# Performance work log

Hardware: AMD Instinct MI355X
Metric: run time of the kernel (lower is better)

The kernel has to match this reference:

```python
import jax, jax.numpy as jnp
import numpy as np

TEMPERATURE = 0.07
COS_EPS = 1e-8  # torch F.cosine_similarity clamps norms at eps=1e-8


def setup_inputs() -> dict:
    key = jax.random.key(0)
    features = jax.random.normal(key, (8192, 1024), dtype=jnp.float32)
    return {"features": features}


def reference(features):
    n = features.shape[0]
    b = n // 2
    # Cosine similarity as normalize + GEMM (equivalent to broadcasted F.cosine_similarity)
    norms = jnp.maximum(jnp.linalg.norm(features, axis=1, keepdims=True), COS_EPS)
    fn = features / norms                      # [N, D]
    sim = (fn @ fn.T) / TEMPERATURE            # [N, N]
    # Mask self-similarity on the diagonal with -inf
    diag = jnp.eye(n, dtype=bool)
    sim = jnp.where(diag, -jnp.inf, sim)
    # labels: positive of i is its paired augmentation (i+b mod n)
    labels = jnp.concatenate([jnp.arange(b) + b, jnp.arange(b)])  # [N]
    # Cross-entropy in one stable pass
    log_probs = jax.nn.log_softmax(sim, axis=1)
    loss = -jnp.mean(log_probs[jnp.arange(n), labels])
    return loss
```

## Files before the change

kernel.cpp:

```cpp
#include <hip/hip_runtime.h>
#include <hip/hip_bf16.h>

#define N_ROWS 8192
#define D_DIM  1024
#define HALF_N 4096
#define N_TILES 2080
#define N_RED  8
constexpr float INV_T = 1.0f / 0.07f;

typedef __attribute__((ext_vector_type(4))) float f32x4;
typedef __attribute__((ext_vector_type(2))) long long2_;

__device__ __forceinline__ void async_ld16(const void* g, void* lds) {
    __builtin_amdgcn_global_load_lds(
        (const __attribute__((address_space(1))) void*)g,
        (__attribute__((address_space(3))) void*)lds,
        16, 0, 0);
}

__device__ __forceinline__ unsigned int pk_fp8x4(float a, float b, float c, float d) {
    int v = __builtin_amdgcn_cvt_pk_fp8_f32(a, b, 0, false);
    v = __builtin_amdgcn_cvt_pk_fp8_f32(c, d, v, true);
    return (unsigned int)v;
}

__global__ __launch_bounds__(256) void norm_kernel(const float* __restrict__ feat,
                                                   unsigned char* __restrict__ fn8,
                                                   float* __restrict__ row_sum,
                                                   unsigned int* __restrict__ done_cnt,
                                                   unsigned int* __restrict__ fin_cnt,
                                                   float* __restrict__ loss_acc) {
    const int w = threadIdx.x >> 6, lane = threadIdx.x & 63;
    const int row = blockIdx.x * 4 + w;
    if (blockIdx.x == 0 && threadIdx.x == 0) {
        *done_cnt = 0u;
        *fin_cnt = 0u;
        *loss_acc = 0.f;
    }
    const float4* src = (const float4*)(feat + (size_t)row * D_DIM);
    float4 v[4];
    float ss = 0.f;
#pragma unroll
    for (int t = 0; t < 4; ++t) {
        v[t] = src[lane + 64 * t];
        ss += v[t].x * v[t].x + v[t].y * v[t].y + v[t].z * v[t].z + v[t].w * v[t].w;
    }
#pragma unroll
    for (int off = 32; off; off >>= 1) ss += __shfl_xor(ss, off);
    float nrm = fmaxf(sqrtf(ss), 1e-8f);
    if (lane == 0) row_sum[row] = 0.f;
    const float inv = 1.0f / nrm;
    unsigned int* dst = (unsigned int*)(fn8 + (size_t)row * D_DIM);
#pragma unroll
    for (int t = 0; t < 4; ++t)
        dst[lane + 64 * t] = pk_fp8x4(v[t].x * inv, v[t].y * inv, v[t].z * inv, v[t].w * inv);
}

__global__ __launch_bounds__(256) void simgemm_kernel(const unsigned char* __restrict__ fn8,
                                                      float* __restrict__ row_sum,
                                                      float* __restrict__ s_target,
                                                      unsigned int* __restrict__ done_cnt,
                                                      unsigned int* __restrict__ fin_cnt,
                                                      float* __restrict__ loss_acc,
                                                      float* __restrict__ out) {
    __shared__ __align__(16) unsigned char As[128 * 64];
    __shared__ __align__(16) unsigned char Bs[128 * 64];
    const int t = blockIdx.x;
    int a = (int)((sqrtf(8.f * (float)t + 1.f) - 1.f) * 0.5f);
    while ((a + 1) * (a + 2) / 2 <= t) ++a;
    while (a * (a + 1) / 2 > t) --a;
    const int I = t - a * (a + 1) / 2;
    const int J = a;
    const int r0 = I * 128, c0 = J * 128;
    const bool isdiag = (I == J);
    const bool haspair = (J == I + 32);

    const int tid = threadIdx.x;
    const int w = tid >> 6, lane = tid & 63;
    const int q = lane >> 4, c16 = lane & 15;
    const int wr = (w >> 1) * 64;
    const int wc = (w & 1) * 64;
    const int wr4 = (w >> 1) * 4;
    const int wc4 = (w & 1) * 4;
    const int srow = lane >> 2;
    const int skoff = ((lane & 3) ^ ((srow >> 1) & 3)) * 16;
    const int lfo = c16 * 64 + ((q ^ ((c16 >> 1) & 3)) * 16);

    const unsigned char* pa0 = fn8 + (size_t)(r0 + w * 32 + srow) * D_DIM + skoff;
    const unsigned char* pa1 = pa0 + 16 * D_DIM;
    const unsigned char* pb0 = fn8 + (size_t)(c0 + w * 32 + srow) * D_DIM + skoff;
    const unsigned char* pb1 = pb0 + 16 * D_DIM;

    f32x4 acc[4][4];
#pragma unroll
    for (int i = 0; i < 4; ++i)
#pragma unroll
        for (int j = 0; j < 4; ++j) acc[i][j] = (f32x4){0.f, 0.f, 0.f, 0.f};

    for (int kt = 0; kt < 16; ++kt) {
        __syncthreads();
        async_ld16(pa0, (void*)&As[(w * 2 + 0) * 1024]);
        async_ld16(pa1, (void*)&As[(w * 2 + 1) * 1024]);
        async_ld16(pb0, (void*)&Bs[(w * 2 + 0) * 1024]);
        async_ld16(pb1, (void*)&Bs[(w * 2 + 1) * 1024]);
        pa0 += 64; pa1 += 64; pb0 += 64; pb1 += 64;
        __syncthreads();

        long2_ af[4], bf[4];
#pragma unroll
        for (int i = 0; i < 4; ++i)
            af[i] = *(const long2_*)&As[(wr4 + i) * 1024 + lfo];
#pragma unroll
        for (int j = 0; j < 4; ++j)
            bf[j] = *(const long2_*)&Bs[(wc4 + j) * 1024 + lfo];
#pragma unroll
        for (int i = 0; i < 4; ++i)
#pragma unroll
            for (int j = 0; j < 4; ++j) {
                acc[i][j] = __builtin_amdgcn_mfma_f32_16x16x32_fp8_fp8(
                    af[i].x, bf[j].x, acc[i][j], 0, 0, 0);
                acc[i][j] = __builtin_amdgcn_mfma_f32_16x16x32_fp8_fp8(
                    af[i].y, bf[j].y, acc[i][j], 0, 0, 0);
            }
    }

    float cs[4] = {0.f, 0.f, 0.f, 0.f};
#pragma unroll
    for (int i = 0; i < 4; ++i) {
        const int growb = r0 + wr + i * 16 + q * 4;
#pragma unroll
        for (int r = 0; r < 4; ++r) {
            const int grow = growb + r;
            float s = 0.f;
#pragma unroll
            for (int j = 0; j < 4; ++j) {
                const int gcol = c0 + wc + j * 16 + c16;
                float sim = acc[i][j][r] * INV_T;
                float e = __expf(sim - INV_T);
                if (isdiag && grow == gcol) e = 0.f;
                if (haspair && gcol == grow + HALF_N) {
                    __hip_atomic_store(&s_target[grow], sim, __ATOMIC_RELAXED,
                                       __HIP_MEMORY_SCOPE_AGENT);
                    __hip_atomic_store(&s_target[gcol], sim, __ATOMIC_RELAXED,
                                       __HIP_MEMORY_SCOPE_AGENT);
                }
                s += e;
                cs[j] += e;
            }
            s += __shfl_xor(s, 1);
            s += __shfl_xor(s, 2);
            s += __shfl_xor(s, 4);
            s += __shfl_xor(s, 8);
            if (c16 == 0) atomicAdd(&row_sum[grow], s);
        }
    }
    if (!isdiag) {
#pragma unroll
        for (int j = 0; j < 4; ++j) {
            float s = cs[j];
            s += __shfl_xor(s, 16);
            s += __shfl_xor(s, 32);
            if (q == 0) atomicAdd(&row_sum[c0 + wc + j * 16 + c16], s);
        }
    }

    __syncthreads();
    __shared__ unsigned int my_ord;
    if (tid == 0)
        my_ord = __hip_atomic_fetch_add(done_cnt, 1u, __ATOMIC_RELAXED,
                                        __HIP_MEMORY_SCOPE_AGENT);
    __syncthreads();
    const unsigned int ord = my_ord;
    if (ord >= N_TILES - N_RED) {
        if (tid == 0) {
            while (__hip_atomic_load(done_cnt, __ATOMIC_RELAXED,
                                     __HIP_MEMORY_SCOPE_AGENT) < N_TILES)
                __builtin_amdgcn_s_sleep(1);
        }
        __syncthreads();
        const int slice = (int)(ord - (N_TILES - N_RED));
        const int base_row = slice * (N_ROWS / N_RED) + tid * 4;
        float rv[4], sv[4];
#pragma unroll
        for (int u = 0; u < 4; ++u) {
            rv[u] = __hip_atomic_load(&row_sum[base_row + u], __ATOMIC_RELAXED,
                                      __HIP_MEMORY_SCOPE_AGENT);
            sv[u] = __hip_atomic_load(&s_target[base_row + u], __ATOMIC_RELAXED,
                                      __HIP_MEMORY_SCOPE_AGENT);
        }
        float local = 0.f;
#pragma unroll
        for (int u = 0; u < 4; ++u)
            local += __logf(rv[u]) - sv[u];
#pragma unroll
        for (int off = 32; off; off >>= 1) local += __shfl_xor(local, off);
        __shared__ float part[4];
        if ((tid & 63) == 0) part[tid >> 6] = local;
        __syncthreads();
        if (tid == 0) {
            float bsum = part[0] + part[1] + part[2] + part[3];
            __hip_atomic_fetch_add(loss_acc, bsum, __ATOMIC_RELAXED,
                                   __HIP_MEMORY_SCOPE_AGENT);
            unsigned int f = __hip_atomic_fetch_add(fin_cnt, 1u, __ATOMIC_ACQ_REL,
                                                    __HIP_MEMORY_SCOPE_AGENT);
            if (f == N_RED - 1) {
                float accv = __hip_atomic_load(loss_acc, __ATOMIC_RELAXED,
                                               __HIP_MEMORY_SCOPE_AGENT);
                out[0] = INV_T + accv * (1.0f / N_ROWS);
            }
        }
    }
}

extern "C" void kernel_launch(void* const* d_in, const int* in_sizes, int n_in,
                              void* d_out, int out_size, void* d_ws, size_t ws_size,
                              hipStream_t stream) {
    const float* feat = (const float*)d_in[0];
    float* out = (float*)d_out;
    char* ws = (char*)d_ws;

    unsigned char* fn8 = (unsigned char*)ws;
    size_t off = (size_t)N_ROWS * D_DIM;
    float* row_sum = (float*)(ws + off);   off += N_ROWS * sizeof(float);
    float* s_target = (float*)(ws + off);  off += N_ROWS * sizeof(float);
    unsigned int* done_cnt = (unsigned int*)(ws + off);  off += sizeof(unsigned int);
    unsigned int* fin_cnt = (unsigned int*)(ws + off);   off += sizeof(unsigned int);
    float* loss_acc = (float*)(ws + off);

    norm_kernel<<<N_ROWS / 4, 256, 0, stream>>>(feat, fn8, row_sum, done_cnt, fin_cnt, loss_acc);
    simgemm_kernel<<<N_TILES, 256, 0, stream>>>(fn8, row_sum, s_target, done_cnt, fin_cnt, loss_acc, out);
}
```

Measured before the change: 142.7 us.

## Use 128x256 tiles with triple-buffered async LDS pipeline and 8 waves

Each block now computes a 128x256 tile of the upper-triangular similarity matrix with 512 threads, so the grid shrinks from 2080 to 1056 blocks. Tile masking is rewritten to handle rectangular tiles that straddle the diagonal. The K loop is software-pipelined with three LDS buffers, raw barriers and explicit waitcnts, and setprio is raised around the MFMA bursts so loads overlap with compute. The aim is fewer barriers per MFMA and hidden global-load latency. The cost is more LDS per block and harder-to-verify synchronisation, and the diagonal tiles do some redundant work.

```diff
diff --git a/kernel.cpp b/kernel.cpp
--- a/kernel.cpp
+++ b/kernel.cpp
@@ -4,7 +4,7 @@
 #define N_ROWS 8192
 #define D_DIM  1024
 #define HALF_N 4096
-#define N_TILES 2080
+#define N_TILES 1056
 #define N_RED  8
 constexpr float INV_T = 1.0f / 0.07f;
 
@@ -56,38 +56,52 @@
         dst[lane + 64 * t] = pk_fp8x4(v[t].x * inv, v[t].y * inv, v[t].z * inv, v[t].w * inv);
 }
 
-__global__ __launch_bounds__(256) void simgemm_kernel(const unsigned char* __restrict__ fn8,
-                                                      float* __restrict__ row_sum,
-                                                      float* __restrict__ s_target,
-                                                      unsigned int* __restrict__ done_cnt,
-                                                      unsigned int* __restrict__ fin_cnt,
-                                                      float* __restrict__ loss_acc,
-                                                      float* __restrict__ out) {
-    __shared__ __align__(16) unsigned char As[128 * 64];
-    __shared__ __align__(16) unsigned char Bs[128 * 64];
+#define BARRIER() do { asm volatile("" ::: "memory"); \
+    __builtin_amdgcn_s_barrier();                      \
+    asm volatile("" ::: "memory"); } while (0)
+
+#define MROW(AF, I_) do { \
+    acc[I_][0] = __builtin_amdgcn_mfma_f32_16x16x32_fp8_fp8(AF.x, bf[0].x, acc[I_][0], 0, 0, 0); \
+    acc[I_][1] = __builtin_amdgcn_mfma_f32_16x16x32_fp8_fp8(AF.x, bf[1].x, acc[I_][1], 0, 0, 0); \
+    acc[I_][2] = __builtin_amdgcn_mfma_f32_16x16x32_fp8_fp8(AF.x, bf[2].x, acc[I_][2], 0, 0, 0); \
+    acc[I_][3] = __builtin_amdgcn_mfma_f32_16x16x32_fp8_fp8(AF.x, bf[3].x, acc[I_][3], 0, 0, 0); \
+    acc[I_][0] = __builtin_amdgcn_mfma_f32_16x16x32_fp8_fp8(AF.y, bf[0].y, acc[I_][0], 0, 0, 0); \
+    acc[I_][1] = __builtin_amdgcn_mfma_f32_16x16x32_fp8_fp8(AF.y, bf[1].y, acc[I_][1], 0, 0, 0); \
+    acc[I_][2] = __builtin_amdgcn_mfma_f32_16x16x32_fp8_fp8(AF.y, bf[2].y, acc[I_][2], 0, 0, 0); \
+    acc[I_][3] = __builtin_amdgcn_mfma_f32_16x16x32_fp8_fp8(AF.y, bf[3].y, acc[I_][3], 0, 0, 0); \
+} while (0)
+
+__global__ __launch_bounds__(512, 4) void simgemm_kernel(const unsigned char* __restrict__ fn8,
+                                                         float* __restrict__ row_sum,
+                                                         float* __restrict__ s_target,
+                                                         unsigned int* __restrict__ done_cnt,
+                                                         unsigned int* __restrict__ fin_cnt,
+                                                         float* __restrict__ loss_acc,
+                                                         float* __restrict__ out) {
+    __shared__ __align__(16) unsigned char As[3][8 * 1024];
+    __shared__ __align__(16) unsigned char Bs[3][16 * 1024];
+
     const int t = blockIdx.x;
-    int a = (int)((sqrtf(8.f * (float)t + 1.f) - 1.f) * 0.5f);
-    while ((a + 1) * (a + 2) / 2 <= t) ++a;
-    while (a * (a + 1) / 2 > t) --a;
-    const int I = t - a * (a + 1) / 2;
-    const int J = a;
-    const int r0 = I * 128, c0 = J * 128;
-    const bool isdiag = (I == J);
-    const bool haspair = (J == I + 32);
+#define CSUM(i) (32 * (i) - ((i) >> 1) * (((i) - 1) >> 1))
+    int I = 64 - (int)sqrtf(fmaxf(4096.f - 4.f * (float)t, 0.f)) - 2;
+    if (I < 0) I = 0;
+    if (I > 63) I = 63;
+    while (CSUM(I + 1) <= t) ++I;
+    while (CSUM(I) > t) --I;
+    const int J = (I >> 1) + (t - CSUM(I));
+    const int r0 = I * 128, c0 = J * 256;
+    const bool haspair = (J == (I >> 1) + (HALF_N / 256));
 
     const int tid = threadIdx.x;
     const int w = tid >> 6, lane = tid & 63;
     const int q = lane >> 4, c16 = lane & 15;
-    const int wr = (w >> 1) * 64;
-    const int wc = (w & 1) * 64;
-    const int wr4 = (w >> 1) * 4;
-    const int wc4 = (w & 1) * 4;
+    const int wm = w >> 2, wn = w & 3;
+    const int wm4 = wm * 4, wn4 = wn * 4;
     const int srow = lane >> 2;
     const int skoff = ((lane & 3) ^ ((srow >> 1) & 3)) * 16;
     const int lfo = c16 * 64 + ((q ^ ((c16 >> 1) & 3)) * 16);
 
-    const unsigned char* pa0 = fn8 + (size_t)(r0 + w * 32 + srow) * D_DIM + skoff;
-    const unsigned char* pa1 = pa0 + 16 * D_DIM;
+    const unsigned char* pa  = fn8 + (size_t)(r0 + w * 16 + srow) * D_DIM + skoff;
     const unsigned char* pb0 = fn8 + (size_t)(c0 + w * 32 + srow) * D_DIM + skoff;
     const unsigned char* pb1 = pb0 + 16 * D_DIM;
 
@@ -97,47 +111,75 @@
 #pragma unroll
         for (int j = 0; j < 4; ++j) acc[i][j] = (f32x4){0.f, 0.f, 0.f, 0.f};
 
+    async_ld16(pa,       &As[0][w * 1024]);
+    async_ld16(pb0,      &Bs[0][(2 * w) * 1024]);
+    async_ld16(pb1,      &Bs[0][(2 * w + 1) * 1024]);
+    async_ld16(pa  + 64, &As[1][w * 1024]);
+    async_ld16(pb0 + 64, &Bs[1][(2 * w) * 1024]);
+    async_ld16(pb1 + 64, &Bs[1][(2 * w + 1) * 1024]);
+    pa += 128; pb0 += 128; pb1 += 128;
+    asm volatile("s_waitcnt vmcnt(3)" ::: "memory");
+    BARRIER();
+
+    int cur = 0;
     for (int kt = 0; kt < 16; ++kt) {
-        __syncthreads();
-        async_ld16(pa0, (void*)&As[(w * 2 + 0) * 1024]);
-        async_ld16(pa1, (void*)&As[(w * 2 + 1) * 1024]);
-        async_ld16(pb0, (void*)&Bs[(w * 2 + 0) * 1024]);
-        async_ld16(pb1, (void*)&Bs[(w * 2 + 1) * 1024]);
-        pa0 += 64; pa1 += 64; pb0 += 64; pb1 += 64;
-        __syncthreads();
-
-        long2_ af[4], bf[4];
-#pragma unroll
-        for (int i = 0; i < 4; ++i)
-            af[i] = *(const long2_*)&As[(wr4 + i) * 1024 + lfo];
-#pragma unroll
-        for (int j = 0; j < 4; ++j)
-            bf[j] = *(const long2_*)&Bs[(wc4 + j) * 1024 + lfo];
-#pragma unroll
-        for (int i = 0; i < 4; ++i)
-#pragma unroll
-            for (int j = 0; j < 4; ++j) {
-                acc[i][j] = __builtin_amdgcn_mfma_f32_16x16x32_fp8_fp8(
-                    af[i].x, bf[j].x, acc[i][j], 0, 0, 0);
-                acc[i][j] = __builtin_amdgcn_mfma_f32_16x16x32_fp8_fp8(
-                    af[i].y, bf[j].y, acc[i][j], 0, 0, 0);
-            }
+        const bool pre = (kt < 14);
+        int nb = cur + 2; if (nb >= 3) nb -= 3;
+        long2_ bf[4], a0, a1;
+        bf[0] = *(const long2_*)&Bs[cur][(wn4 + 0) * 1024 + lfo];
+        bf[1] = *(const long2_*)&Bs[cur][(wn4 + 1) * 1024 + lfo];
+        bf[2] = *(const long2_*)&Bs[cur][(wn4 + 2) * 1024 + lfo];
+        bf[3] = *(const long2_*)&Bs[cur][(wn4 + 3) * 1024 + lfo];
+        a0 = *(const long2_*)&As[cur][(wm4 + 0) * 1024 + lfo];
+        a1 = *(const long2_*)&As[cur][(wm4 + 1) * 1024 + lfo];
+        if (pre) {
+            async_ld16(pa,  &As[nb][w * 1024]);
+            async_ld16(pb0, &Bs[nb][(2 * w) * 1024]);
+        }
+        BARRIER();
+        asm volatile("s_waitcnt lgkmcnt(0)" ::: "memory");
+        __builtin_amdgcn_s_setprio(1);
+        MROW(a0, 0);
+        MROW(a1, 1);
+        __builtin_amdgcn_s_setprio(0);
+        BARRIER();
+        a0 = *(const long2_*)&As[cur][(wm4 + 2) * 1024 + lfo];
+        a1 = *(const long2_*)&As[cur][(wm4 + 3) * 1024 + lfo];
+        if (pre) {
+            async_ld16(pb1, &Bs[nb][(2 * w + 1) * 1024]);
+            pa += 64; pb0 += 64; pb1 += 64;
+        }
+        BARRIER();
+        asm volatile("s_waitcnt lgkmcnt(0)" ::: "memory");
+        __builtin_amdgcn_s_setprio(1);
+        MROW(a0, 2);
+        MROW(a1, 3);
+        __builtin_amdgcn_s_setprio(0);
+        if (kt < 14) {
+            asm volatile("s_waitcnt vmcnt(3)" ::: "memory");
+            BARRIER();
+        } else if (kt == 14) {
+            asm volatile("s_waitcnt vmcnt(0)" ::: "memory");
+            BARRIER();
+        }
+        cur = (cur == 2) ? 0 : cur + 1;
     }
 
     float cs[4] = {0.f, 0.f, 0.f, 0.f};
 #pragma unroll
     for (int i = 0; i < 4; ++i) {
-        const int growb = r0 + wr + i * 16 + q * 4;
+        const int growb = r0 + wm * 64 + i * 16 + q * 4;
 #pragma unroll
         for (int r = 0; r < 4; ++r) {
             const int grow = growb + r;
             float s = 0.f;
 #pragma unroll
             for (int j = 0; j < 4; ++j) {
-                const int gcol = c0 + wc + j * 16 + c16;
+                const int gcol = c0 + wn * 64 + j * 16 + c16;
                 float sim = acc[i][j][r] * INV_T;
                 float e = __expf(sim - INV_T);
-                if (isdiag && grow == gcol) e = 0.f;
+                const bool same128 = (((grow ^ gcol) >> 7) == 0);
+                if (grow == gcol || (!same128 && grow > gcol)) e = 0.f;
                 if (haspair && gcol == grow + HALF_N) {
                     __hip_atomic_store(&s_target[grow], sim, __ATOMIC_RELAXED,
                                        __HIP_MEMORY_SCOPE_AGENT);
@@ -145,7 +187,7 @@
                                        __HIP_MEMORY_SCOPE_AGENT);
                 }
                 s += e;
-                cs[j] += e;
+                cs[j] += same128 ? 0.f : e;
             }
             s += __shfl_xor(s, 1);
             s += __shfl_xor(s, 2);
@@ -154,14 +196,12 @@
             if (c16 == 0) atomicAdd(&row_sum[grow], s);
         }
     }
-    if (!isdiag) {
-#pragma unroll
-        for (int j = 0; j < 4; ++j) {
-            float s = cs[j];
-            s += __shfl_xor(s, 16);
-            s += __shfl_xor(s, 32);
-            if (q == 0) atomicAdd(&row_sum[c0 + wc + j * 16 + c16], s);
-        }
+#pragma unroll
+    for (int j = 0; j < 4; ++j) {
+        float s = cs[j];
+        s += __shfl_xor(s, 16);
+        s += __shfl_xor(s, 32);
+        if (q == 0) atomicAdd(&row_sum[c0 + wn * 64 + j * 16 + c16], s);
     }
 
     __syncthreads();
@@ -179,26 +219,25 @@
         }
         __syncthreads();
         const int slice = (int)(ord - (N_TILES - N_RED));
-        const int base_row = slice * (N_ROWS / N_RED) + tid * 4;
-        float rv[4], sv[4];
-#pragma unroll
-        for (int u = 0; u < 4; ++u) {
-            rv[u] = __hip_atomic_load(&row_sum[base_row + u], __ATOMIC_RELAXED,
-                                      __HIP_MEMORY_SCOPE_AGENT);
-            sv[u] = __hip_atomic_load(&s_target[base_row + u], __ATOMIC_RELAXED,
-                                      __HIP_MEMORY_SCOPE_AGENT);
-        }
-        float local = 0.f;
-#pragma unroll
-        for (int u = 0; u < 4; ++u)
-            local += __logf(rv[u]) - sv[u];
+        const int base_row = slice * (N_ROWS / N_RED) + tid * 2;
+        float rv0 = __hip_atomic_load(&row_sum[base_row + 0], __ATOMIC_RELAXED,
+                                      __HIP_MEMORY_SCOPE_AGENT);
+        float rv1 = __hip_atomic_load(&row_sum[base_row + 1], __ATOMIC_RELAXED,
+                                      __HIP_MEMORY_SCOPE_AGENT);
+        float sv0 = __hip_atomic_load(&s_target[base_row + 0], __ATOMIC_RELAXED,
+                                      __HIP_MEMORY_SCOPE_AGENT);
+        float sv1 = __hip_atomic_load(&s_target[base_row + 1], __ATOMIC_RELAXED,
+                                      __HIP_MEMORY_SCOPE_AGENT);
+        float local = __logf(rv0) - sv0 + __logf(rv1) - sv1;
 #pragma unroll
         for (int off = 32; off; off >>= 1) local += __shfl_xor(local, off);
-        __shared__ float part[4];
-        if ((tid & 63) == 0) part[tid >> 6] = local;
+        __shared__ float part[8];
+        if ((tid & 63) == 0) part[w] = local;
         __syncthreads();
         if (tid == 0) {
-            float bsum = part[0] + part[1] + part[2] + part[3];
+            float bsum = 0.f;
+#pragma unroll
+            for (int k = 0; k < 8; ++k) bsum += part[k];
             __hip_atomic_fetch_add(loss_acc, bsum, __ATOMIC_RELAXED,
                                    __HIP_MEMORY_SCOPE_AGENT);
             unsigned int f = __hip_atomic_fetch_add(fin_cnt, 1u, __ATOMIC_ACQ_REL,
@@ -228,5 +267,5 @@
     float* loss_acc = (float*)(ws + off);
 
     norm_kernel<<<N_ROWS / 4, 256, 0, stream>>>(feat, fn8, row_sum, done_cnt, fin_cnt, loss_acc);
-    simgemm_kernel<<<N_TILES, 256, 0, stream>>>(fn8, row_sum, s_target, done_cnt, fin_cnt, loss_acc, out);
-}
+    simgemm_kernel<<<N_TILES, 512, 0, stream>>>(fn8, row_sum, s_target, done_cnt, fin_cnt, loss_acc, out);
+}
```

New measurement: 153.6 us. +7.6%, slower.

## Triple-buffer LDS tiles with async prefetch and split MFMA phases

Applied to the files above, without the earlier changes.

Replaces the single-buffered LDS load/compute loop with a three-stage ring buffer that keeps two k-tiles of async global-to-LDS loads in flight, with manual vmcnt waits and one barrier per iteration instead of two. The MFMA work is split into two half phases with interleaved LDS fragment reads and raised wave priority, and occupancy is hinted via launch bounds. This aims to hide global load latency behind the matrix math. It triples LDS use per block, which may limit occupancy, and depends on hand-written waitcnt correctness.

```diff
diff --git a/kernel.cpp b/kernel.cpp
--- a/kernel.cpp
+++ b/kernel.cpp
@@ -56,15 +56,30 @@
         dst[lane + 64 * t] = pk_fp8x4(v[t].x * inv, v[t].y * inv, v[t].z * inv, v[t].w * inv);
 }
 
-__global__ __launch_bounds__(256) void simgemm_kernel(const unsigned char* __restrict__ fn8,
-                                                      float* __restrict__ row_sum,
-                                                      float* __restrict__ s_target,
-                                                      unsigned int* __restrict__ done_cnt,
-                                                      unsigned int* __restrict__ fin_cnt,
-                                                      float* __restrict__ loss_acc,
-                                                      float* __restrict__ out) {
-    __shared__ __align__(16) unsigned char As[128 * 64];
-    __shared__ __align__(16) unsigned char Bs[128 * 64];
+#define BARRIER() do { asm volatile("" ::: "memory"); \
+    __builtin_amdgcn_s_barrier();                      \
+    asm volatile("" ::: "memory"); } while (0)
+
+#define MROW(AF, I_) do { \
+    acc[I_][0] = __builtin_amdgcn_mfma_f32_16x16x32_fp8_fp8(AF.x, bf[0].x, acc[I_][0], 0, 0, 0); \
+    acc[I_][1] = __builtin_amdgcn_mfma_f32_16x16x32_fp8_fp8(AF.x, bf[1].x, acc[I_][1], 0, 0, 0); \
+    acc[I_][2] = __builtin_amdgcn_mfma_f32_16x16x32_fp8_fp8(AF.x, bf[2].x, acc[I_][2], 0, 0, 0); \
+    acc[I_][3] = __builtin_amdgcn_mfma_f32_16x16x32_fp8_fp8(AF.x, bf[3].x, acc[I_][3], 0, 0, 0); \
+    acc[I_][0] = __builtin_amdgcn_mfma_f32_16x16x32_fp8_fp8(AF.y, bf[0].y, acc[I_][0], 0, 0, 0); \
+    acc[I_][1] = __builtin_amdgcn_mfma_f32_16x16x32_fp8_fp8(AF.y, bf[1].y, acc[I_][1], 0, 0, 0); \
+    acc[I_][2] = __builtin_amdgcn_mfma_f32_16x16x32_fp8_fp8(AF.y, bf[2].y, acc[I_][2], 0, 0, 0); \
+    acc[I_][3] = __builtin_amdgcn_mfma_f32_16x16x32_fp8_fp8(AF.y, bf[3].y, acc[I_][3], 0, 0, 0); \
+} while (0)
+
+__global__ __launch_bounds__(256, 3) void simgemm_kernel(const unsigned char* __restrict__ fn8,
+                                                         float* __restrict__ row_sum,
+                                                         float* __restrict__ s_target,
+                                                         unsigned int* __restrict__ done_cnt,
+                                                         unsigned int* __restrict__ fin_cnt,
+                                                         float* __restrict__ loss_acc,
+                                                         float* __restrict__ out) {
+    __shared__ __align__(16) unsigned char As[3][8 * 1024];
+    __shared__ __align__(16) unsigned char Bs[3][8 * 1024];
     const int t = blockIdx.x;
     int a = (int)((sqrtf(8.f * (float)t + 1.f) - 1.f) * 0.5f);
     while ((a + 1) * (a + 2) / 2 <= t) ++a;
@@ -97,31 +112,54 @@
 #pragma unroll
         for (int j = 0; j < 4; ++j) acc[i][j] = (f32x4){0.f, 0.f, 0.f, 0.f};
 
+    async_ld16(pa0,      &As[0][(w * 2 + 0) * 1024]);
+    async_ld16(pa1,      &As[0][(w * 2 + 1) * 1024]);
+    async_ld16(pb0,      &Bs[0][(w * 2 + 0) * 1024]);
+    async_ld16(pb1,      &Bs[0][(w * 2 + 1) * 1024]);
+    async_ld16(pa0 + 64, &As[1][(w * 2 + 0) * 1024]);
+    async_ld16(pa1 + 64, &As[1][(w * 2 + 1) * 1024]);
+    async_ld16(pb0 + 64, &Bs[1][(w * 2 + 0) * 1024]);
+    async_ld16(pb1 + 64, &Bs[1][(w * 2 + 1) * 1024]);
+    asm volatile("s_waitcnt vmcnt(4)" ::: "memory");
+    BARRIER();
+
+    int cur = 0;
     for (int kt = 0; kt < 16; ++kt) {
-        __syncthreads();
-        async_ld16(pa0, (void*)&As[(w * 2 + 0) * 1024]);
-        async_ld16(pa1, (void*)&As[(w * 2 + 1) * 1024]);
-        async_ld16(pb0, (void*)&Bs[(w * 2 + 0) * 1024]);
-        async_ld16(pb1, (void*)&Bs[(w * 2 + 1) * 1024]);
-        pa0 += 64; pa1 += 64; pb0 += 64; pb1 += 64;
-        __syncthreads();
-
-        long2_ af[4], bf[4];
-#pragma unroll
-        for (int i = 0; i < 4; ++i)
-            af[i] = *(const long2_*)&As[(wr4 + i) * 1024 + lfo];
-#pragma unroll
-        for (int j = 0; j < 4; ++j)
-            bf[j] = *(const long2_*)&Bs[(wc4 + j) * 1024 + lfo];
-#pragma unroll
-        for (int i = 0; i < 4; ++i)
-#pragma unroll
-            for (int j = 0; j < 4; ++j) {
-                acc[i][j] = __builtin_amdgcn_mfma_f32_16x16x32_fp8_fp8(
-                    af[i].x, bf[j].x, acc[i][j], 0, 0, 0);
-                acc[i][j] = __builtin_amdgcn_mfma_f32_16x16x32_fp8_fp8(
-                    af[i].y, bf[j].y, acc[i][j], 0, 0, 0);
-            }
+        int nb = cur + 2; if (nb >= 3) nb -= 3;
+        long2_ bf[4], a0, a1;
+        bf[0] = *(const long2_*)&Bs[cur][(wc4 + 0) * 1024 + lfo];
+        bf[1] = *(const long2_*)&Bs[cur][(wc4 + 1) * 1024 + lfo];
+        bf[2] = *(const long2_*)&Bs[cur][(wc4 + 2) * 1024 + lfo];
+        bf[3] = *(const long2_*)&Bs[cur][(wc4 + 3) * 1024 + lfo];
+        a0 = *(const long2_*)&As[cur][(wr4 + 0) * 1024 + lfo];
+        a1 = *(const long2_*)&As[cur][(wr4 + 1) * 1024 + lfo];
+        if (kt < 14) {
+            const int off = (kt + 2) * 64;
+            async_ld16(pa0 + off, &As[nb][(w * 2 + 0) * 1024]);
+            async_ld16(pa1 + off, &As[nb][(w * 2 + 1) * 1024]);
+            async_ld16(pb0 + off, &Bs[nb][(w * 2 + 0) * 1024]);
+            async_ld16(pb1 + off, &Bs[nb][(w * 2 + 1) * 1024]);
+        }
+        asm volatile("s_waitcnt lgkmcnt(0)" ::: "memory");
+        __builtin_amdgcn_s_setprio(1);
+        MROW(a0, 0);
+        MROW(a1, 1);
+        __builtin_amdgcn_s_setprio(0);
+        a0 = *(const long2_*)&As[cur][(wr4 + 2) * 1024 + lfo];
+        a1 = *(const long2_*)&As[cur][(wr4 + 3) * 1024 + lfo];
+        asm volatile("s_waitcnt lgkmcnt(0)" ::: "memory");
+        __builtin_amdgcn_s_setprio(1);
+        MROW(a0, 2);
+        MROW(a1, 3);
+        __builtin_amdgcn_s_setprio(0);
+        if (kt < 14) {
+            asm volatile("s_waitcnt vmcnt(4)" ::: "memory");
+            BARRIER();
+        } else if (kt == 14) {
+            asm volatile("s_waitcnt vmcnt(0)" ::: "memory");
+            BARRIER();
+        }
+        cur = (cur == 2) ? 0 : cur + 1;
     }
 
     float cs[4] = {0.f, 0.f, 0.f, 0.f};
```

After: 142.2 us. No clear change (-0.4%).

## Switch FP8 GEMM to 32x32x64 scaled MFMA with 128-wide K tiles

Applied to the files above, without the earlier changes.

Replaces the 16x16x32 fp8 MFMA tiles with the gfx950 mfma_scale 32x32x64 f8f6f4 instruction (unit scales), changes the per-wave accumulator layout to 2x2 32x32 tiles and doubles the K step per LDS stage to 128 bytes with a new XOR swizzle. This halves the number of barrier-separated K iterations and cuts MFMA instruction count, aiming at higher matrix throughput. The epilogue reductions are rewritten for the 32x32 output layout, which risks layout or swizzle errors and raises LDS use to 32KB.

```diff
diff --git a/kernel.cpp b/kernel.cpp
--- a/kernel.cpp
+++ b/kernel.cpp
@@ -8,8 +8,10 @@
 #define N_RED  8
 constexpr float INV_T = 1.0f / 0.07f;
 
-typedef __attribute__((ext_vector_type(4))) float f32x4;
-typedef __attribute__((ext_vector_type(2))) long long2_;
+typedef __attribute__((ext_vector_type(4)))  float f32x4;
+typedef __attribute__((ext_vector_type(16))) float f32x16;
+typedef __attribute__((ext_vector_type(4)))  int   i32x4;
+typedef __attribute__((ext_vector_type(8)))  int   i32x8;
 
 __device__ __forceinline__ void async_ld16(const void* g, void* lds) {
     __builtin_amdgcn_global_load_lds(
@@ -23,6 +25,18 @@
     v = __builtin_amdgcn_cvt_pk_fp8_f32(c, d, v, true);
     return (unsigned int)v;
 }
+
+__device__ __forceinline__ i32x8 ld_frag(const unsigned char* rowbase, int lo, int hi) {
+    i32x4 L = *(const i32x4*)(rowbase + lo);
+    i32x4 H = *(const i32x4*)(rowbase + hi);
+    i32x8 r;
+    r[0] = L[0]; r[1] = L[1]; r[2] = L[2]; r[3] = L[3];
+    r[4] = H[0]; r[5] = H[1]; r[6] = H[2]; r[7] = H[3];
+    return r;
+}
+
+#define MXMFMA(AF, BF, ACC) ACC = __builtin_amdgcn_mfma_scale_f32_32x32x64_f8f6f4( \
+        AF, BF, ACC, 0, 0, 0, 0x7F7F7F7F, 0, 0x7F7F7F7F)
 
 __global__ __launch_bounds__(256) void norm_kernel(const float* __restrict__ feat,
                                                    unsigned char* __restrict__ fn8,
@@ -63,8 +77,8 @@
                                                       unsigned int* __restrict__ fin_cnt,
                                                       float* __restrict__ loss_acc,
                                                       float* __restrict__ out) {
-    __shared__ __align__(16) unsigned char As[128 * 64];
-    __shared__ __align__(16) unsigned char Bs[128 * 64];
+    __shared__ __align__(16) unsigned char As[128 * 128];
+    __shared__ __align__(16) unsigned char Bs[128 * 128];
     const int t = blockIdx.x;
     int a = (int)((sqrtf(8.f * (float)t + 1.f) - 1.f) * 0.5f);
     while ((a + 1) * (a + 2) / 2 <= t) ++a;
@@ -77,65 +91,62 @@
 
     const int tid = threadIdx.x;
     const int w = tid >> 6, lane = tid & 63;
-    const int q = lane >> 4, c16 = lane & 15;
     const int wr = (w >> 1) * 64;
     const int wc = (w & 1) * 64;
-    const int wr4 = (w >> 1) * 4;
-    const int wc4 = (w & 1) * 4;
-    const int srow = lane >> 2;
-    const int skoff = ((lane & 3) ^ ((srow >> 1) & 3)) * 16;
-    const int lfo = c16 * 64 + ((q ^ ((c16 >> 1) & 3)) * 16);
-
-    const unsigned char* pa0 = fn8 + (size_t)(r0 + w * 32 + srow) * D_DIM + skoff;
-    const unsigned char* pa1 = pa0 + 16 * D_DIM;
-    const unsigned char* pb0 = fn8 + (size_t)(c0 + w * 32 + srow) * D_DIM + skoff;
-    const unsigned char* pb1 = pb0 + 16 * D_DIM;
-
-    f32x4 acc[4][4];
-#pragma unroll
-    for (int i = 0; i < 4; ++i)
-#pragma unroll
-        for (int j = 0; j < 4; ++j) acc[i][j] = (f32x4){0.f, 0.f, 0.f, 0.f};
-
-    for (int kt = 0; kt < 16; ++kt) {
-        __syncthreads();
-        async_ld16(pa0, (void*)&As[(w * 2 + 0) * 1024]);
-        async_ld16(pa1, (void*)&As[(w * 2 + 1) * 1024]);
-        async_ld16(pb0, (void*)&Bs[(w * 2 + 0) * 1024]);
-        async_ld16(pb1, (void*)&Bs[(w * 2 + 1) * 1024]);
-        pa0 += 64; pa1 += 64; pb0 += 64; pb1 += 64;
-        __syncthreads();
-
-        long2_ af[4], bf[4];
-#pragma unroll
-        for (int i = 0; i < 4; ++i)
-            af[i] = *(const long2_*)&As[(wr4 + i) * 1024 + lfo];
-#pragma unroll
-        for (int j = 0; j < 4; ++j)
-            bf[j] = *(const long2_*)&Bs[(wc4 + j) * 1024 + lfo];
-#pragma unroll
-        for (int i = 0; i < 4; ++i)
-#pragma unroll
-            for (int j = 0; j < 4; ++j) {
-                acc[i][j] = __builtin_amdgcn_mfma_f32_16x16x32_fp8_fp8(
-                    af[i].x, bf[j].x, acc[i][j], 0, 0, 0);
-                acc[i][j] = __builtin_amdgcn_mfma_f32_16x16x32_fp8_fp8(
-                    af[i].y, bf[j].y, acc[i][j], 0, 0, 0);
-            }
-    }
-
-    float cs[4] = {0.f, 0.f, 0.f, 0.f};
-#pragma unroll
-    for (int i = 0; i < 4; ++i) {
-        const int growb = r0 + wr + i * 16 + q * 4;
-#pragma unroll
-        for (int r = 0; r < 4; ++r) {
-            const int grow = growb + r;
+
+    const int srow = lane >> 3;
+    const int slog = ((lane & 7) ^ srow) * 16;
+    const unsigned char* pa = fn8 + (size_t)(r0 + w * 32 + srow) * D_DIM + slog;
+    const unsigned char* pb = fn8 + (size_t)(c0 + w * 32 + srow) * D_DIM + slog;
+
+    const int fr = lane & 31;
+    const int h = lane >> 5;
+    const int fs = fr & 7;
+    const unsigned char* pA0 = &As[(((w >> 1) * 2 + 0) * 4096) + fr * 128];
+    const unsigned char* pA1 = &As[(((w >> 1) * 2 + 1) * 4096) + fr * 128];
+    const unsigned char* pB0 = &Bs[(((w & 1) * 2 + 0) * 4096) + fr * 128];
+    const unsigned char* pB1 = &Bs[(((w & 1) * 2 + 1) * 4096) + fr * 128];
+
+    f32x16 acc[2][2] = {};
+
+    for (int kt = 0; kt < 8; ++kt) {
+        __syncthreads();
+#pragma unroll
+        for (int i = 0; i < 4; ++i) {
+            async_ld16(pa + (size_t)i * 8 * D_DIM, &As[w * 4096 + i * 1024]);
+            async_ld16(pb + (size_t)i * 8 * D_DIM, &Bs[w * 4096 + i * 1024]);
+        }
+        pa += 128; pb += 128;
+        __syncthreads();
+
+#pragma unroll
+        for (int k64 = 0; k64 < 2; ++k64) {
+            const int lo = ((4 * k64 + 2 * h) ^ fs) * 16;
+            const int hi = ((4 * k64 + 2 * h + 1) ^ fs) * 16;
+            i32x8 a0 = ld_frag(pA0, lo, hi);
+            i32x8 a1 = ld_frag(pA1, lo, hi);
+            i32x8 b0 = ld_frag(pB0, lo, hi);
+            i32x8 b1 = ld_frag(pB1, lo, hi);
+            MXMFMA(a0, b0, acc[0][0]);
+            MXMFMA(a0, b1, acc[0][1]);
+            MXMFMA(a1, b0, acc[1][0]);
+            MXMFMA(a1, b1, acc[1][1]);
+        }
+    }
+
+    const int colL = lane & 31;
+    float cs[2] = {0.f, 0.f};
+#pragma unroll
+    for (int ti = 0; ti < 2; ++ti) {
+#pragma unroll
+        for (int reg = 0; reg < 16; ++reg) {
+            const int rowL = (reg & 3) + 8 * (reg >> 2) + 4 * h;
+            const int grow = r0 + wr + ti * 32 + rowL;
             float s = 0.f;
 #pragma unroll
-            for (int j = 0; j < 4; ++j) {
-                const int gcol = c0 + wc + j * 16 + c16;
-                float sim = acc[i][j][r] * INV_T;
+            for (int tj = 0; tj < 2; ++tj) {
+                const int gcol = c0 + wc + tj * 32 + colL;
+                float sim = acc[ti][tj][reg] * INV_T;
                 float e = __expf(sim - INV_T);
                 if (isdiag && grow == gcol) e = 0.f;
                 if (haspair && gcol == grow + HALF_N) {
@@ -145,22 +156,21 @@
                                        __HIP_MEMORY_SCOPE_AGENT);
                 }
                 s += e;
-                cs[j] += e;
+                cs[tj] += e;
             }
             s += __shfl_xor(s, 1);
             s += __shfl_xor(s, 2);
             s += __shfl_xor(s, 4);
             s += __shfl_xor(s, 8);
-            if (c16 == 0) atomicAdd(&row_sum[grow], s);
+            s += __shfl_xor(s, 16);
+            if (colL == 0) atomicAdd(&row_sum[grow], s);
         }
     }
     if (!isdiag) {
 #pragma unroll
-        for (int j = 0; j < 4; ++j) {
-            float s = cs[j];
-            s += __shfl_xor(s, 16);
-            s += __shfl_xor(s, 32);
-            if (q == 0) atomicAdd(&row_sum[c0 + wc + j * 16 + c16], s);
+        for (int tj = 0; tj < 2; ++tj) {
+            float s = cs[tj] + __shfl_xor(cs[tj], 32);
+            if (h == 0) atomicAdd(&row_sum[c0 + wc + tj * 32 + colL], s);
         }
     }
 
```

After: 148.6 us. 1.04x slower.
